# Optimization experiments

Hardware: AMD Instinct MI355X
Metric: run time of the kernel (lower is better)

## Reference

```python
import jax, jax.numpy as jnp
import numpy as np

B, S, HID = 1, 2048, 4096
H, KV, D, R = 32, 8, 128, 64   # heads, kv heads, head_dim, rotary_dim
EPS = 1e-6
THETA = 10000.0


def setup_inputs() -> dict:
    key = jax.random.key(0)
    ks = jax.random.split(key, 6)
    sc = 0.02
    return {
        'hidden_states': jax.random.normal(ks[0], (B, S, HID), jnp.float32),
        'Wq': jax.random.normal(ks[1], (H * D, HID), jnp.float32) * sc,
        'Wk': jax.random.normal(ks[2], (KV * D, HID), jnp.float32) * sc,
        'Wv': jax.random.normal(ks[3], (KV * D, HID), jnp.float32) * sc,
        'Wo': jax.random.normal(ks[4], (HID, H * D), jnp.float32) * sc,
        'q_norm_w': jnp.ones((H * D,), jnp.float32),
        'k_norm_w': jnp.ones((KV * D,), jnp.float32),
        'position_ids': jnp.broadcast_to(jnp.arange(S, dtype=jnp.int64)[None, :], (B, S)),
    }


def _rms_norm(x, w):
    xf = x.astype(jnp.float32)
    var = jnp.mean(xf * xf, axis=-1, keepdims=True)
    return (w * (xf * jax.lax.rsqrt(var + EPS))).astype(x.dtype)


def _rotate_half(x):
    x1, x2 = x[..., : R // 2], x[..., R // 2:]
    return jnp.concatenate((-x2, x1), axis=-1)


def reference(hidden_states, Wq, Wk, Wv, Wo, q_norm_w, k_norm_w, position_ids):
    x = hidden_states
    # projections (torch Linear: y = x @ W^T)
    q = jnp.einsum('bsd,od->bso', x, Wq)                      # [B,S,H*D]
    k = jnp.einsum('bsd,od->bso', x, Wk)                      # [B,S,KV*D]
    v = jnp.einsum('bsd,od->bso', x, Wv).reshape(B, S, KV, D)
    # QK RMSNorm over flattened head dims
    q = _rms_norm(q, q_norm_w).reshape(B, S, H, D)
    k = _rms_norm(k, k_norm_w).reshape(B, S, KV, D)
    # partial RoPE: rotary_dim=R out of head_dim=D
    inv_freq = 1.0 / (THETA ** (jnp.arange(0, R, 2, dtype=jnp.float32) / R))  # [R/2]
    freqs = position_ids.astype(jnp.float32)[..., None] * inv_freq            # [B,S,R/2]
    emb = jnp.concatenate((freqs, freqs), axis=-1)                            # [B,S,R]
    cos = jnp.cos(emb)[:, :, None, :]                                         # [B,S,1,R]
    sin = jnp.sin(emb)[:, :, None, :]
    q_rot = q[..., :R] * cos + _rotate_half(q[..., :R]) * sin
    k_rot = k[..., :R] * cos + _rotate_half(k[..., :R]) * sin
    q = jnp.concatenate((q_rot, q[..., R:]), axis=-1)
    k = jnp.concatenate((k_rot, k[..., R:]), axis=-1)
    # GQA repeat_kv
    G = H // KV
    k = jnp.repeat(k, G, axis=2)  # [B,S,H,D]
    v = jnp.repeat(v, G, axis=2)
    # attention with causal mask, softmax in fp32
    scaling = D ** -0.5
    scores = jnp.einsum('bqhd,bkhd->bhqk', q, k) * scaling    # [B,H,S,S]
    causal = jnp.tril(jnp.ones((S, S), dtype=bool))
    scores = jnp.where(causal[None, None], scores, jnp.finfo(jnp.float32).min)
    attn = jax.nn.softmax(scores.astype(jnp.float32), axis=-1).astype(q.dtype)
    out = jnp.einsum('bhqk,bkhd->bqhd', attn, v).reshape(B, S, H * D)
    return jnp.einsum('bso,do->bsd', out, Wo)
```

## Files before the change

### kernel.cpp

```cpp
#include <hip/hip_runtime.h>
#include <hip/hip_bf16.h>
#include <math.h>

typedef __bf16 bf16;
typedef __bf16 bf16x8 __attribute__((ext_vector_type(8)));
typedef float f32x4 __attribute__((ext_vector_type(4)));

#define S_LEN 2048
#define HID_D 4096
#define NH 32
#define NKV 8
#define HD 128
#define SCALE_LOG2 (0.08838834764831843f * 1.4426950408889634f)

__device__ __forceinline__ void gload_lds16(const void* g, void* lds) {
  __builtin_amdgcn_global_load_lds((__attribute__((address_space(1))) void*)g,
                                   (__attribute__((address_space(3))) void*)lds, 16, 0, 0);
}

#define MEMFENCE asm volatile("" ::: "memory")

__global__ __launch_bounds__(256) void cvt_kernel(const float* __restrict__ in,
                                                  bf16* __restrict__ out, int n8) {
  int i = blockIdx.x * blockDim.x + threadIdx.x;
  int stride = gridDim.x * blockDim.x;
  for (; i < n8; i += stride) {
    const float4* p = (const float4*)in + 2 * (size_t)i;
    float4 a = p[0], b = p[1];
    bf16x8 o;
    o[0] = (bf16)a.x; o[1] = (bf16)a.y; o[2] = (bf16)a.z; o[3] = (bf16)a.w;
    o[4] = (bf16)b.x; o[5] = (bf16)b.y; o[6] = (bf16)b.z; o[7] = (bf16)b.w;
    *((bf16x8*)out + i) = o;
  }
}

template <int BM, int BN>
__global__ __launch_bounds__(512, 2) void gemm_s(const bf16* __restrict__ A,
                                                 const bf16* __restrict__ B,
                                                 float* __restrict__ C,
                                                 int N, int Kfull, int T) {
  constexpr int MFr = BM / 32;
  constexpr int NFr = BN / 64;
  constexpr int NL = (BM + BN) / 64;
  constexpr int TILE = (BM + BN) * 128;

  __shared__ __align__(16) char lds[2 * TILE];
  const int t = threadIdx.x, l = t & 63, w = t >> 6;
  const int wr = w >> 2, wc = w & 3;
  const int l15 = l & 15, lg = l >> 4;

  const int nwg = gridDim.x * gridDim.y;
  const int lin = blockIdx.y * gridDim.x + blockIdx.x;
  const int swz = (lin & 7) * (nwg >> 3) + (lin >> 3);
  const int n0 = (swz % gridDim.x) * BN;
  const int m0 = (swz / gridDim.x) * BM;

  auto stage = [&](int d, int tau) {
    char* dst = lds + d * TILE;
    const size_t kpos = (size_t)tau * 64;
#pragma unroll
    for (int i = 0; i < NL; i++) {
      int q = i * 512 + t;
      int r = q >> 3;
      int c = (q & 7) ^ (r & 7);
      const bf16* src = (i * 512 < BM * 8)
                            ? (A + (size_t)(m0 + r) * Kfull)
                            : (B + (size_t)(n0 + (r - BM)) * Kfull);
      gload_lds16(src + kpos + c * 8, dst + q * 16);
    }
  };

  f32x4 acc[MFr][NFr] = {};

  stage(0, 0);
  asm volatile("s_waitcnt vmcnt(0)" ::: "memory");
  MEMFENCE; __builtin_amdgcn_s_barrier(); MEMFENCE;

  for (int tau = 0; tau < T; tau++) {
    const int d = tau & 1;
    if (tau + 1 < T) stage(d ^ 1, tau + 1);

    const char* Ab = lds + d * TILE;
    const char* Bb = Ab + BM * 128;
    bf16x8 a[MFr][2], b[NFr][2];
#pragma unroll
    for (int mf = 0; mf < MFr; mf++) {
      const int row = wr * (BM / 2) + mf * 16 + l15;
#pragma unroll
      for (int ks = 0; ks < 2; ks++)
        a[mf][ks] = *(const bf16x8*)(Ab + row * 128 + (((ks * 4 + lg) ^ (row & 7)) << 4));
    }
#pragma unroll
    for (int nf = 0; nf < NFr; nf++) {
      const int row = wc * (BN / 4) + nf * 16 + l15;
#pragma unroll
      for (int ks = 0; ks < 2; ks++)
        b[nf][ks] = *(const bf16x8*)(Bb + row * 128 + (((ks * 4 + lg) ^ (row & 7)) << 4));
    }
#pragma unroll
    for (int mf = 0; mf < MFr; mf++)
#pragma unroll
      for (int nf = 0; nf < NFr; nf++)
#pragma unroll
        for (int ks = 0; ks < 2; ks++)
          acc[mf][nf] = __builtin_amdgcn_mfma_f32_16x16x32_bf16(a[mf][ks], b[nf][ks],
                                                               acc[mf][nf], 0, 0, 0);

    asm volatile("s_waitcnt vmcnt(0)" ::: "memory");
    MEMFENCE; __builtin_amdgcn_s_barrier(); MEMFENCE;
  }

#pragma unroll
  for (int mf = 0; mf < MFr; mf++) {
    int row = m0 + wr * (BM / 2) + mf * 16 + lg * 4;
#pragma unroll
    for (int nf = 0; nf < NFr; nf++) {
      int col = n0 + wc * (BN / 4) + nf * 16 + l15;
      float* Cp = C + (size_t)row * N + col;
#pragma unroll
      for (int rr = 0; rr < 4; rr++) Cp[(size_t)rr * N] = acc[mf][nf][rr];
    }
  }
}

__global__ __launch_bounds__(256) void vt_kernel(const float* __restrict__ QKV,
                                                 bf16* __restrict__ Vt) {
  __shared__ __align__(16) float tile[64][68];
  const int s0 = blockIdx.x * 64, d0 = blockIdx.y * 64;
  const int t = threadIdx.x;
#pragma unroll
  for (int i = 0; i < 4; i++) {
    int row = i * 16 + (t >> 4);
    int c4 = t & 15;
    float4 v = *(const float4*)(QKV + (size_t)(s0 + row) * 6144 + 5120 + d0 + c4 * 4);
    *(float4*)&tile[row][c4 * 4] = v;
  }
  __syncthreads();
#pragma unroll
  for (int i = 0; i < 2; i++) {
    int slot = i * 256 + t;
    int dr = slot >> 3, ch = slot & 7;
    bf16x8 o;
#pragma unroll
    for (int j = 0; j < 8; j++) o[j] = (bf16)tile[ch * 8 + j][dr];
    *(bf16x8*)(Vt + (size_t)(d0 + dr) * S_LEN + s0 + ch * 8) = o;
  }
}

__global__ __launch_bounds__(256) void prep_kernel(const float* __restrict__ QKV,
                                                   const float* __restrict__ qw,
                                                   const float* __restrict__ kw,
                                                   const int* __restrict__ pos_ids,
                                                   bf16* __restrict__ Qb,
                                                   bf16* __restrict__ Kb) {
  __shared__ __align__(16) float row[5120];
  __shared__ float cs[64];
  __shared__ float red[8];
  const int s = blockIdx.x, t = threadIdx.x;

  const float4* src = (const float4*)(QKV + (size_t)s * 6144);
#pragma unroll
  for (int i = 0; i < 5; i++) ((float4*)row)[t + i * 256] = src[t + i * 256];

  if (t < 32) {
    float p = (float)pos_ids[s];
    float ang = p * powf(10000.0f, -(float)t * (1.0f / 32.0f));
    float sn, cn;
    sincosf(ang, &sn, &cn);
    cs[t] = cn;
    cs[32 + t] = sn;
  }
  __syncthreads();

  float aq = 0.f, ak = 0.f;
  for (int i = t; i < 4096; i += 256) { float v = row[i]; aq += v * v; }
  for (int i = 4096 + t; i < 5120; i += 256) { float v = row[i]; ak += v * v; }
#pragma unroll
  for (int off = 32; off; off >>= 1) {
    aq += __shfl_down(aq, off);
    ak += __shfl_down(ak, off);
  }
  if ((t & 63) == 0) { red[t >> 6] = aq; red[4 + (t >> 6)] = ak; }
  __syncthreads();
  const float scq = rsqrtf((red[0] + red[1] + red[2] + red[3]) * (1.0f / 4096.0f) + 1e-6f);
  const float sck = rsqrtf((red[4] + red[5] + red[6] + red[7]) * (1.0f / 1024.0f) + 1e-6f);

  for (int e = t; e < 4096; e += 256) {
    int d = e & 127;
    int hh = e >> 7;
    float val = row[e] * scq * qw[e];
    float o;
    if (d < 32)       o = val * cs[d] - (row[e + 32] * scq * qw[e + 32]) * cs[32 + d];
    else if (d < 64)  o = val * cs[d - 32] + (row[e - 32] * scq * qw[e - 32]) * cs[d];
    else              o = val;
    Qb[((size_t)hh * S_LEN + s) * HD + d] = (bf16)o;
  }
  for (int e = t; e < 1024; e += 256) {
    int d = e & 127;
    int hh = e >> 7;
    int ri = 4096 + e;
    float val = row[ri] * sck * kw[e];
    float o;
    if (d < 32)       o = val * cs[d] - (row[ri + 32] * sck * kw[e + 32]) * cs[32 + d];
    else if (d < 64)  o = val * cs[d - 32] + (row[ri - 32] * sck * kw[e - 32]) * cs[d];
    else              o = val;
    Kb[((size_t)hh * S_LEN + s) * HD + d] = (bf16)o;
  }
}

__global__ __launch_bounds__(256, 2) void attn_kernel(const bf16* __restrict__ Qb,
                                                      const bf16* __restrict__ Kb,
                                                      const bf16* __restrict__ Vt,
                                                      bf16* __restrict__ Ctx) {
  __shared__ __align__(16) char KB[2][16384];
  __shared__ __align__(16) char VB[2][16384];
  __shared__ __align__(16) char PB[8192];
  const int t = threadIdx.x, l = t & 63, w = t >> 6;
  const int l15 = l & 15, lg = l >> 4;
  const int pairc = blockIdx.x >> 5;
  const int h = blockIdx.x & 31;

  const bf16* Kh = Kb + (size_t)(h >> 2) * S_LEN * HD;
  const bf16* Vh = Vt + (size_t)(h >> 2) * HD * S_LEN;
  char* Pw = PB + w * 2048;

  const int kj0 = t & 15;
  const int vj0 = t & 7;

  auto stageK = [&](int buf, int kvbase) {
#pragma unroll
    for (int i = 0; i < 4; i++) {
      int r = (i * 256 + t) >> 4;
      const bf16* src = Kh + (size_t)(kvbase + r) * HD + ((kj0 ^ (r & 7)) << 3);
      gload_lds16(src, KB[buf] + (i * 256 + w * 64) * 16);
    }
  };
  auto stageV = [&](int buf, int kvbase) {
#pragma unroll
    for (int i = 0; i < 4; i++) {
      int r = (i * 256 + t) >> 3;
      const bf16* src = Vh + (size_t)r * S_LEN + kvbase + ((vj0 ^ (r & 7)) << 3);
      gload_lds16(src, VB[buf] + (i * 256 + w * 64) * 16);
    }
  };

#pragma unroll
  for (int phase = 0; phase < 2; phase++) {
    const int chunk = (phase == 0) ? pairc : (31 - pairc);
    const int ktiles = chunk + 1;
    const int q0 = chunk * 64 + w * 16;

    const bf16* Qh = Qb + ((size_t)h * S_LEN + q0) * HD;
    bf16x8 qf[4];
#pragma unroll
    for (int kk = 0; kk < 4; kk++)
      qf[kk] = *(const bf16x8*)(Qh + (size_t)l15 * HD + kk * 32 + lg * 8);

    stageK(0, 0);
    stageV(0, 0);

    f32x4 O[8] = {};
    float m[4], lsum[4];
#pragma unroll
    for (int r = 0; r < 4; r++) { m[r] = -1e30f; lsum[r] = 0.f; }

    for (int tt = 0; tt < ktiles; tt++) {
      const int cur = tt & 1;
      const int kv0 = tt * 64;
      const char* Kcur = KB[cur];
      const bool hasnext = (tt + 1 < ktiles);

      asm volatile("s_waitcnt vmcnt(0)" ::: "memory");
      MEMFENCE;
      __builtin_amdgcn_s_barrier();
      MEMFENCE;

      f32x4 sc[4];
#pragma unroll
      for (int g = 0; g < 4; g++) sc[g] = (f32x4){0.f, 0.f, 0.f, 0.f};
#pragma unroll
      for (int g = 0; g < 4; g++) {
        const int r = g * 16 + l15;
        const char* Krow = Kcur + r * 256;
        const int sw = (r & 7);
#pragma unroll
        for (int kk = 0; kk < 4; kk++) {
          bf16x8 kf = *(const bf16x8*)(Krow + (((kk * 4 + lg) ^ sw) << 4));
          sc[g] = __builtin_amdgcn_mfma_f32_16x16x32_bf16(qf[kk], kf, sc[g], 0, 0, 0);
        }
      }

      if (hasnext) {
        stageK(cur ^ 1, kv0 + 64);
        stageV(cur ^ 1, kv0 + 64);
      }

      const bool needmask = (kv0 + 63 > q0);
      float sv[4][4];
#pragma unroll
      for (int g = 0; g < 4; g++)
#pragma unroll
        for (int r = 0; r < 4; r++) {
          float x = sc[g][r] * SCALE_LOG2;
          if (needmask) {
            int kv = kv0 + g * 16 + l15;
            int qr = q0 + lg * 4 + r;
            if (kv > qr) x = -1e30f;
          }
          sv[g][r] = x;
        }
      float al[4];
#pragma unroll
      for (int r = 0; r < 4; r++) {
        float x = fmaxf(fmaxf(sv[0][r], sv[1][r]), fmaxf(sv[2][r], sv[3][r]));
        x = fmaxf(x, __shfl_xor(x, 1));
        x = fmaxf(x, __shfl_xor(x, 2));
        x = fmaxf(x, __shfl_xor(x, 4));
        x = fmaxf(x, __shfl_xor(x, 8));
        float mn = fmaxf(m[r], x);
        al[r] = exp2f(m[r] - mn);
        m[r] = mn;
      }
#pragma unroll
      for (int g = 0; g < 4; g++)
#pragma unroll
        for (int r = 0; r < 4; r++) sv[g][r] = exp2f(sv[g][r] - m[r]);
#pragma unroll
      for (int r = 0; r < 4; r++) {
        float x = (sv[0][r] + sv[1][r]) + (sv[2][r] + sv[3][r]);
        x += __shfl_xor(x, 1);
        x += __shfl_xor(x, 2);
        x += __shfl_xor(x, 4);
        x += __shfl_xor(x, 8);
        lsum[r] = lsum[r] * al[r] + x;
      }
#pragma unroll
      for (int dt = 0; dt < 8; dt++)
#pragma unroll
        for (int r = 0; r < 4; r++) O[dt][r] *= al[r];

#pragma unroll
      for (int g = 0; g < 4; g++)
#pragma unroll
        for (int r = 0; r < 4; r++) {
          int prow = lg * 4 + r;
          int pbyte = prow * 128 + (((g * 16 + l15) * 2) ^ ((prow & 7) << 4));
          *(bf16*)(Pw + pbyte) = (bf16)sv[g][r];
        }
      asm volatile("s_waitcnt lgkmcnt(0)" ::: "memory");
      bf16x8 pa[2];
#pragma unroll
      for (int ks = 0; ks < 2; ks++)
        pa[ks] = *(const bf16x8*)(Pw + l15 * 128 + (((ks * 4 + lg) ^ (l15 & 7)) << 4));

#pragma unroll
      for (int ks = 0; ks < 2; ks++)
#pragma unroll
        for (int dt = 0; dt < 8; dt++) {
          const int r = dt * 16 + l15;
          bf16x8 vf = *(const bf16x8*)(VB[cur] + r * 128 + (((ks * 4 + lg) ^ (r & 7)) << 4));
          O[dt] = __builtin_amdgcn_mfma_f32_16x16x32_bf16(pa[ks], vf, O[dt], 0, 0, 0);
        }
    }

    MEMFENCE;
    __builtin_amdgcn_s_barrier();
    MEMFENCE;

#pragma unroll
    for (int r = 0; r < 4; r++) {
      float inv = 1.0f / lsum[r];
      bf16* Cp = Ctx + (size_t)(q0 + lg * 4 + r) * HID_D + h * HD + l15;
#pragma unroll
      for (int dt = 0; dt < 8; dt++) Cp[dt * 16] = (bf16)(O[dt][r] * inv);
    }
  }
}

extern "C" void kernel_launch(void* const* d_in, const int* in_sizes, int n_in,
                              void* d_out, int out_size, void* d_ws, size_t ws_size,
                              hipStream_t stream) {
  const float* X  = (const float*)d_in[0];
  const float* Wq = (const float*)d_in[1];
  const float* Wk = (const float*)d_in[2];
  const float* Wv = (const float*)d_in[3];
  const float* Wo = (const float*)d_in[4];
  const float* qw = (const float*)d_in[5];
  const float* kw = (const float*)d_in[6];
  const int* pos  = (const int*)d_in[7];

  char* ws = (char*)d_ws;
  bf16* Xb    = (bf16*)ws;
  bf16* Wqkvb = (bf16*)(ws + (16ll << 20));
  bf16* Wob   = Wqkvb;
  float* QKV  = (float*)(ws + (64ll << 20));
  bf16* Ctx   = (bf16*)(ws + (96ll << 20));
  bf16* Qb    = (bf16*)(ws + (112ll << 20));
  bf16* Kb    = (bf16*)(ws + (128ll << 20));
  bf16* Vt    = (bf16*)(ws + (132ll << 20));

  cvt_kernel<<<2048, 256, 0, stream>>>(X, Xb, S_LEN * HID_D / 8);
  cvt_kernel<<<2048, 256, 0, stream>>>(Wq, Wqkvb, 4096 * 4096 / 8);
  cvt_kernel<<<512, 256, 0, stream>>>(Wk, Wqkvb + 4096 * 4096, 1024 * 4096 / 8);
  cvt_kernel<<<512, 256, 0, stream>>>(Wv, Wqkvb + 5120 * 4096, 1024 * 4096 / 8);

  gemm_s<128, 384><<<dim3(16, 16), 512, 0, stream>>>(Xb, Wqkvb, QKV, 6144, HID_D, 64);

  cvt_kernel<<<2048, 256, 0, stream>>>(Wo, Wob, 4096 * 4096 / 8);

  vt_kernel<<<dim3(32, 16), 256, 0, stream>>>(QKV, Vt);
  prep_kernel<<<S_LEN, 256, 0, stream>>>(QKV, qw, kw, pos, Qb, Kb);

  attn_kernel<<<dim3(512), 256, 0, stream>>>(Qb, Kb, Vt, Ctx);

  gemm_s<128, 256><<<dim3(16, 16), 512, 0, stream>>>(Ctx, Wob, (float*)d_out,
                                                     HID_D, HID_D, 64);
}
```

Baseline: 354.3 us.

## Process 32 query rows per wave and skip softmax rescale when max is stable

```diff
diff --git a/kernel.cpp b/kernel.cpp
--- a/kernel.cpp
+++ b/kernel.cpp
@@ -214,7 +214,7 @@
                                                       bf16* __restrict__ Ctx) {
   __shared__ __align__(16) char KB[2][16384];
   __shared__ __align__(16) char VB[2][16384];
-  __shared__ __align__(16) char PB[8192];
+  __shared__ __align__(16) char PB[16384];
   const int t = threadIdx.x, l = t & 63, w = t >> 6;
   const int l15 = l & 15, lg = l >> 4;
   const int pairc = blockIdx.x >> 5;
@@ -222,7 +222,7 @@
 
   const bf16* Kh = Kb + (size_t)(h >> 2) * S_LEN * HD;
   const bf16* Vh = Vt + (size_t)(h >> 2) * HD * S_LEN;
-  char* Pw = PB + w * 2048;
+  char* Pw = PB + w * 4096;
 
   const int kj0 = t & 15;
   const int vj0 = t & 7;
@@ -246,23 +246,27 @@
 
 #pragma unroll
   for (int phase = 0; phase < 2; phase++) {
-    const int chunk = (phase == 0) ? pairc : (31 - pairc);
-    const int ktiles = chunk + 1;
-    const int q0 = chunk * 64 + w * 16;
+    const int chunk = (phase == 0) ? pairc : (15 - pairc);
+    const int ktiles = 2 * chunk + 2;
+    const int q0 = chunk * 128 + w * 32;
 
     const bf16* Qh = Qb + ((size_t)h * S_LEN + q0) * HD;
-    bf16x8 qf[4];
-#pragma unroll
-    for (int kk = 0; kk < 4; kk++)
-      qf[kk] = *(const bf16x8*)(Qh + (size_t)l15 * HD + kk * 32 + lg * 8);
+    bf16x8 qf[2][4];
+#pragma unroll
+    for (int rt = 0; rt < 2; rt++)
+#pragma unroll
+      for (int kk = 0; kk < 4; kk++)
+        qf[rt][kk] = *(const bf16x8*)(Qh + (size_t)(rt * 16 + l15) * HD + kk * 32 + lg * 8);
 
     stageK(0, 0);
     stageV(0, 0);
 
-    f32x4 O[8] = {};
-    float m[4], lsum[4];
-#pragma unroll
-    for (int r = 0; r < 4; r++) { m[r] = -1e30f; lsum[r] = 0.f; }
+    f32x4 O[2][8] = {};
+    float m[2][4], lsum[2][4];
+#pragma unroll
+    for (int rt = 0; rt < 2; rt++)
+#pragma unroll
+      for (int r = 0; r < 4; r++) { m[rt][r] = -1e30f; lsum[rt][r] = 0.f; }
 
     for (int tt = 0; tt < ktiles; tt++) {
       const int cur = tt & 1;
@@ -275,9 +279,11 @@
       __builtin_amdgcn_s_barrier();
       MEMFENCE;
 
-      f32x4 sc[4];
-#pragma unroll
-      for (int g = 0; g < 4; g++) sc[g] = (f32x4){0.f, 0.f, 0.f, 0.f};
+      f32x4 sc[2][4];
+#pragma unroll
+      for (int rt = 0; rt < 2; rt++)
+#pragma unroll
+        for (int g = 0; g < 4; g++) sc[rt][g] = (f32x4){0.f, 0.f, 0.f, 0.f};
 #pragma unroll
       for (int g = 0; g < 4; g++) {
         const int r = g * 16 + l15;
@@ -286,7 +292,8 @@
 #pragma unroll
         for (int kk = 0; kk < 4; kk++) {
           bf16x8 kf = *(const bf16x8*)(Krow + (((kk * 4 + lg) ^ sw) << 4));
-          sc[g] = __builtin_amdgcn_mfma_f32_16x16x32_bf16(qf[kk], kf, sc[g], 0, 0, 0);
+          sc[0][g] = __builtin_amdgcn_mfma_f32_16x16x32_bf16(qf[0][kk], kf, sc[0][g], 0, 0, 0);
+          sc[1][g] = __builtin_amdgcn_mfma_f32_16x16x32_bf16(qf[1][kk], kf, sc[1][g], 0, 0, 0);
         }
       }
 
@@ -296,62 +303,88 @@
       }
 
       const bool needmask = (kv0 + 63 > q0);
-      float sv[4][4];
-#pragma unroll
-      for (int g = 0; g < 4; g++)
+      float sv[2][4][4];
+#pragma unroll
+      for (int rt = 0; rt < 2; rt++)
+#pragma unroll
+        for (int g = 0; g < 4; g++)
+#pragma unroll
+          for (int r = 0; r < 4; r++) {
+            float x = sc[rt][g][r] * SCALE_LOG2;
+            if (needmask) {
+              int kv = kv0 + g * 16 + l15;
+              int qr = q0 + rt * 16 + lg * 4 + r;
+              if (kv > qr) x = -1e30f;
+            }
+            sv[rt][g][r] = x;
+          }
+      float pmax[2][4];
+#pragma unroll
+      for (int rt = 0; rt < 2; rt++)
 #pragma unroll
         for (int r = 0; r < 4; r++) {
-          float x = sc[g][r] * SCALE_LOG2;
-          if (needmask) {
-            int kv = kv0 + g * 16 + l15;
-            int qr = q0 + lg * 4 + r;
-            if (kv > qr) x = -1e30f;
+          float x = fmaxf(fmaxf(sv[rt][0][r], sv[rt][1][r]), fmaxf(sv[rt][2][r], sv[rt][3][r]));
+          x = fmaxf(x, __shfl_xor(x, 1));
+          x = fmaxf(x, __shfl_xor(x, 2));
+          x = fmaxf(x, __shfl_xor(x, 4));
+          x = fmaxf(x, __shfl_xor(x, 8));
+          pmax[rt][r] = x;
+        }
+      int ok = 1;
+#pragma unroll
+      for (int rt = 0; rt < 2; rt++)
+#pragma unroll
+        for (int r = 0; r < 4; r++) ok &= (pmax[rt][r] <= m[rt][r] + 8.0f);
+      if (!__all(ok)) {
+#pragma unroll
+        for (int rt = 0; rt < 2; rt++)
+#pragma unroll
+          for (int r = 0; r < 4; r++) {
+            float mn = fmaxf(m[rt][r], pmax[rt][r]);
+            float al = exp2f(m[rt][r] - mn);
+            m[rt][r] = mn;
+            lsum[rt][r] *= al;
+#pragma unroll
+            for (int dt = 0; dt < 8; dt++) O[rt][dt][r] *= al;
           }
-          sv[g][r] = x;
+      }
+#pragma unroll
+      for (int rt = 0; rt < 2; rt++)
+#pragma unroll
+        for (int g = 0; g < 4; g++)
+#pragma unroll
+          for (int r = 0; r < 4; r++) sv[rt][g][r] = exp2f(sv[rt][g][r] - m[rt][r]);
+#pragma unroll
+      for (int rt = 0; rt < 2; rt++)
+#pragma unroll
+        for (int r = 0; r < 4; r++) {
+          float x = (sv[rt][0][r] + sv[rt][1][r]) + (sv[rt][2][r] + sv[rt][3][r]);
+          x += __shfl_xor(x, 1);
+          x += __shfl_xor(x, 2);
+          x += __shfl_xor(x, 4);
+          x += __shfl_xor(x, 8);
+          lsum[rt][r] += x;
         }
-      float al[4];
-#pragma unroll
-      for (int r = 0; r < 4; r++) {
-        float x = fmaxf(fmaxf(sv[0][r], sv[1][r]), fmaxf(sv[2][r], sv[3][r]));
-        x = fmaxf(x, __shfl_xor(x, 1));
-        x = fmaxf(x, __shfl_xor(x, 2));
-        x = fmaxf(x, __shfl_xor(x, 4));
-        x = fmaxf(x, __shfl_xor(x, 8));
-        float mn = fmaxf(m[r], x);
-        al[r] = exp2f(m[r] - mn);
-        m[r] = mn;
-      }
-#pragma unroll
-      for (int g = 0; g < 4; g++)
-#pragma unroll
-        for (int r = 0; r < 4; r++) sv[g][r] = exp2f(sv[g][r] - m[r]);
-#pragma unroll
-      for (int r = 0; r < 4; r++) {
-        float x = (sv[0][r] + sv[1][r]) + (sv[2][r] + sv[3][r]);
-        x += __shfl_xor(x, 1);
-        x += __shfl_xor(x, 2);
-        x += __shfl_xor(x, 4);
-        x += __shfl_xor(x, 8);
-        lsum[r] = lsum[r] * al[r] + x;
-      }
-#pragma unroll
-      for (int dt = 0; dt < 8; dt++)
-#pragma unroll
-        for (int r = 0; r < 4; r++) O[dt][r] *= al[r];
-
-#pragma unroll
-      for (int g = 0; g < 4; g++)
-#pragma unroll
-        for (int r = 0; r < 4; r++) {
-          int prow = lg * 4 + r;
-          int pbyte = prow * 128 + (((g * 16 + l15) * 2) ^ ((prow & 7) << 4));
-          *(bf16*)(Pw + pbyte) = (bf16)sv[g][r];
+
+#pragma unroll
+      for (int rt = 0; rt < 2; rt++)
+#pragma unroll
+        for (int g = 0; g < 4; g++)
+#pragma unroll
+          for (int r = 0; r < 4; r++) {
+            int prow = rt * 16 + lg * 4 + r;
+            int pbyte = prow * 128 + (((g * 16 + l15) * 2) ^ ((prow & 7) << 4));
+            *(bf16*)(Pw + pbyte) = (bf16)sv[rt][g][r];
+          }
+      asm volatile("s_waitcnt lgkmcnt(0)" ::: "memory");
+      bf16x8 pa[2][2];
+#pragma unroll
+      for (int rt = 0; rt < 2; rt++)
+#pragma unroll
+        for (int ks = 0; ks < 2; ks++) {
+          int prow = rt * 16 + l15;
+          pa[rt][ks] = *(const bf16x8*)(Pw + prow * 128 + (((ks * 4 + lg) ^ (prow & 7)) << 4));
         }
-      asm volatile("s_waitcnt lgkmcnt(0)" ::: "memory");
-      bf16x8 pa[2];
-#pragma unroll
-      for (int ks = 0; ks < 2; ks++)
-        pa[ks] = *(const bf16x8*)(Pw + l15 * 128 + (((ks * 4 + lg) ^ (l15 & 7)) << 4));
 
 #pragma unroll
       for (int ks = 0; ks < 2; ks++)
@@ -359,7 +392,8 @@
         for (int dt = 0; dt < 8; dt++) {
           const int r = dt * 16 + l15;
           bf16x8 vf = *(const bf16x8*)(VB[cur] + r * 128 + (((ks * 4 + lg) ^ (r & 7)) << 4));
-          O[dt] = __builtin_amdgcn_mfma_f32_16x16x32_bf16(pa[ks], vf, O[dt], 0, 0, 0);
+          O[0][dt] = __builtin_amdgcn_mfma_f32_16x16x32_bf16(pa[0][ks], vf, O[0][dt], 0, 0, 0);
+          O[1][dt] = __builtin_amdgcn_mfma_f32_16x16x32_bf16(pa[1][ks], vf, O[1][dt], 0, 0, 0);
         }
     }
 
@@ -368,12 +402,14 @@
     MEMFENCE;
 
 #pragma unroll
-    for (int r = 0; r < 4; r++) {
-      float inv = 1.0f / lsum[r];
-      bf16* Cp = Ctx + (size_t)(q0 + lg * 4 + r) * HID_D + h * HD + l15;
-#pragma unroll
-      for (int dt = 0; dt < 8; dt++) Cp[dt * 16] = (bf16)(O[dt][r] * inv);
-    }
+    for (int rt = 0; rt < 2; rt++)
+#pragma unroll
+      for (int r = 0; r < 4; r++) {
+        float inv = 1.0f / lsum[rt][r];
+        bf16* Cp = Ctx + (size_t)(q0 + rt * 16 + lg * 4 + r) * HID_D + h * HD + l15;
+#pragma unroll
+        for (int dt = 0; dt < 8; dt++) Cp[dt * 16] = (bf16)(O[rt][dt][r] * inv);
+      }
   }
 }
 
@@ -411,7 +447,7 @@
   vt_kernel<<<dim3(32, 16), 256, 0, stream>>>(QKV, Vt);
   prep_kernel<<<S_LEN, 256, 0, stream>>>(QKV, qw, kw, pos, Qb, Kb);
 
-  attn_kernel<<<dim3(512), 256, 0, stream>>>(Qb, Kb, Vt, Ctx);
+  attn_kernel<<<dim3(256), 256, 0, stream>>>(Qb, Kb, Vt, Ctx);
 
   gemm_s<128, 256><<<dim3(16, 16), 512, 0, stream>>>(Ctx, Wob, (float*)d_out,
                                                      HID_D, HID_D, 64);
```

New measurement: 375.0 us. 1.06x slower.
